# Optimization experiments

Measured on AMD Instinct MI355X. Metric: run time of the kernel, lower is better.

Reference implementation:

```python
import jax, jax.numpy as jnp
import numpy as np

B, T, C = 2, 2048, 1024
NH, HS = 16, 64  # n_heads, head_size; NH*HS == C


def setup_inputs() -> dict:
    key = jax.random.key(0)
    k1, k2, k3 = jax.random.split(key, 3)
    x = jax.random.normal(k1, (B, T, C), dtype=jnp.float32)
    W_attn = jax.random.normal(k2, (C, 3 * C), dtype=jnp.float32) * (C ** -0.5)
    b_attn = jax.random.normal(k3, (3 * C,), dtype=jnp.float32) * 0.02
    return {"x": x, "W_attn": W_attn, "b_attn": b_attn}


def reference(x, W_attn, b_attn):
    Bv, Tv, Cv = x.shape
    qkv = x @ W_attn + b_attn                       # [B,T,3C]
    q, k, v = jnp.split(qkv, 3, axis=-1)            # each [B,T,C]
    q = q.reshape(Bv, Tv, NH, HS)
    k = k.reshape(Bv, Tv, NH, HS)
    v = v.reshape(Bv, Tv, NH, HS)
    scale = HS ** -0.5
    wei = jnp.einsum('bqhd,bkhd->bhqk', q, k) * scale  # [B,H,T,T]
    causal = jnp.tril(jnp.ones((Tv, Tv), dtype=bool))
    wei = jnp.where(causal[None, None], wei, -jnp.inf)
    wei = jax.nn.softmax(wei, axis=-1)
    # dropout layers are identity in eval mode
    out = jnp.einsum('bhqk,bkhd->bqhd', wei, v)     # [B,T,H,HS]
    return out.reshape(Bv, Tv, Cv)
```

## Files before the change

### kernel.cpp

```cpp
#include <hip/hip_runtime.h>
#include <hip/hip_bf16.h>
#include <math.h>

#define BB   2
#define TT   2048
#define CC   1024
#define NH   16
#define HS   64
#define N3C  3072
#define MM   4096

typedef __attribute__((ext_vector_type(8))) short bf16x8;
typedef __attribute__((ext_vector_type(4))) float f32x4;

#define NINF (-__builtin_inff())
#define QSCALE 0.125f

__device__ __forceinline__ unsigned short f2bf(float f) {
    unsigned int u = __builtin_bit_cast(unsigned int, f);
    unsigned int r = u + 0x7fffu + ((u >> 16) & 1u);
    return (unsigned short)(r >> 16);
}

__device__ __forceinline__ unsigned short f2bf_fast(float f) {
    unsigned int u = __builtin_bit_cast(unsigned int, f);
    return (unsigned short)((u + 0x8000u) >> 16);
}

__device__ __forceinline__ void gl_lds16(const unsigned short* g, unsigned short* l) {
    __builtin_amdgcn_global_load_lds(
        (const __attribute__((address_space(1))) unsigned int*)g,
        (__attribute__((address_space(3))) unsigned int*)l, 16, 0, 0);
}

__global__ __launch_bounds__(256) void k_cast(const float* __restrict__ x,
                                              unsigned short* __restrict__ xb) {
    int i = (blockIdx.x * 256 + threadIdx.x) * 4;
    float4 v = *(const float4*)(x + i);
    ushort4 o;
    o.x = f2bf(v.x); o.y = f2bf(v.y); o.z = f2bf(v.z); o.w = f2bf(v.w);
    *(ushort4*)(xb + i) = o;
}

__global__ __launch_bounds__(256) void k_transpose_w(const float* __restrict__ W,
                                                     unsigned short* __restrict__ Wt) {
    __shared__ float tile[32][33];
    const int n0 = blockIdx.x * 32;
    const int k0 = blockIdx.y * 32;
    const int t = threadIdx.x;
    {
        int kr = t >> 3, ns = (t & 7) * 4;
        float4 v = *(const float4*)(W + (size_t)(k0 + kr) * N3C + n0 + ns);
        tile[kr][ns + 0] = v.x; tile[kr][ns + 1] = v.y;
        tile[kr][ns + 2] = v.z; tile[kr][ns + 3] = v.w;
    }
    __syncthreads();
    {
        int nr = t >> 3, ks = (t & 7) * 4;
        ushort4 o;
        o.x = f2bf(tile[ks + 0][nr]);
        o.y = f2bf(tile[ks + 1][nr]);
        o.z = f2bf(tile[ks + 2][nr]);
        o.w = f2bf(tile[ks + 3][nr]);
        *(ushort4*)(Wt + (size_t)(n0 + nr) * CC + k0 + ks) = o;
    }
}

#define EPS 72

__global__ __launch_bounds__(256) void k_gemm_qkv(const unsigned short* __restrict__ xb,
                                                  const unsigned short* __restrict__ wt,
                                                  const float* __restrict__ bias,
                                                  unsigned short* __restrict__ qb,
                                                  unsigned short* __restrict__ kb,
                                                  unsigned short* __restrict__ vt) {
    __shared__ unsigned short sA[128 * 32];
    __shared__ unsigned short sB[128 * 32];
    __shared__ unsigned short sE[4 * 64 * EPS];
    const int t = threadIdx.x;
    const int wave = t >> 6, lane = t & 63;
    const int quad = lane >> 4, c16 = lane & 15;
    const int wm = wave >> 1, wn = wave & 1;
    const int m0 = blockIdx.y * 128;
    const int n0 = blockIdx.x * 128;
    const int sel = n0 >> 10;

    f32x4 acc[4][4];
#pragma unroll
    for (int i = 0; i < 4; ++i)
#pragma unroll
        for (int j = 0; j < 4; ++j) acc[i][j] = f32x4{0, 0, 0, 0};

    const int srow = wave * 16 + (lane >> 2);
    const int scol = (lane & 3) * 8;
    const unsigned short* gA = xb + (size_t)(m0 + srow) * CC + scol;
    const unsigned short* gB = wt + (size_t)(n0 + srow) * CC + scol;
    unsigned short* lA = sA + wave * 512 + lane * 8;
    unsigned short* lB = sB + wave * 512 + lane * 8;

    for (int k0 = 0; k0 < CC; k0 += 32) {
        __syncthreads();
        gl_lds16(gA + k0, lA);
        gl_lds16(gA + k0 + (size_t)64 * CC, lA + 2048);
        gl_lds16(gB + k0, lB);
        gl_lds16(gB + k0 + (size_t)64 * CC, lB + 2048);
        __syncthreads();
        bf16x8 a[4], b[4];
#pragma unroll
        for (int rt = 0; rt < 4; ++rt)
            a[rt] = *(const bf16x8*)(sA + (wm * 64 + rt * 16 + c16) * 32 + quad * 8);
#pragma unroll
        for (int ct = 0; ct < 4; ++ct)
            b[ct] = *(const bf16x8*)(sB + (wn * 64 + ct * 16 + c16) * 32 + quad * 8);
#pragma unroll
        for (int rt = 0; rt < 4; ++rt)
#pragma unroll
            for (int ct = 0; ct < 4; ++ct)
                acc[rt][ct] = __builtin_amdgcn_mfma_f32_16x16x32_bf16(b[ct], a[rt], acc[rt][ct], 0, 0, 0);
    }

    const int head = ((n0 + wn * 64) >> 6) & 15;
    const int bh = (m0 >> 11) * NH + head;
    const int tbase = (m0 & 2047) + wm * 64;
    if (sel < 2) {
        unsigned short* dst = (sel == 0) ? qb : kb;
        const float sc = (sel == 0) ? QSCALE : 1.0f;
        unsigned short* ew = sE + wave * (64 * EPS);
#pragma unroll
        for (int ct = 0; ct < 4; ++ct) {
            const float4 bv4 = *(const float4*)(bias + n0 + wn * 64 + ct * 16 + quad * 4);
            const int d0 = ct * 16 + quad * 4;
#pragma unroll
            for (int rt = 0; rt < 4; ++rt) {
                ushort4 pk;
                pk.x = f2bf((acc[rt][ct][0] + bv4.x) * sc);
                pk.y = f2bf((acc[rt][ct][1] + bv4.y) * sc);
                pk.z = f2bf((acc[rt][ct][2] + bv4.z) * sc);
                pk.w = f2bf((acc[rt][ct][3] + bv4.w) * sc);
                *(ushort4*)(ew + (rt * 16 + c16) * EPS + d0) = pk;
            }
        }
        const size_t gbase = ((size_t)bh * TT + tbase) * HS;
#pragma unroll
        for (int i = 0; i < 8; ++i) {
            const int trow = i * 8 + (lane >> 3);
            bf16x8 row = *(const bf16x8*)(ew + trow * EPS + (lane & 7) * 8);
            *(bf16x8*)(dst + gbase + (size_t)trow * HS + (lane & 7) * 8) = row;
        }
    } else {
#pragma unroll
        for (int ct = 0; ct < 4; ++ct) {
            const float4 bv4 = *(const float4*)(bias + n0 + wn * 64 + ct * 16 + quad * 4);
#pragma unroll
            for (int r = 0; r < 4; ++r) {
                const int d = ct * 16 + quad * 4 + r;
                const float bv = ((const float*)&bv4)[r];
#pragma unroll
                for (int rt = 0; rt < 4; ++rt) {
                    const int tt = tbase + rt * 16 + c16;
                    vt[((size_t)bh * HS + d) * TT + tt] = f2bf(acc[rt][ct][r] + bv);
                }
            }
        }
    }
}

#define SPP 72

__global__ __launch_bounds__(64) void k_attn(const unsigned short* __restrict__ qb,
                                             const unsigned short* __restrict__ kb,
                                             const unsigned short* __restrict__ vt,
                                             float* __restrict__ out) {
    __shared__ unsigned short sP[32 * SPP];

    const int lane = threadIdx.x;
    const int quad = lane >> 4, c16 = lane & 15;
    const int qblk = 63 - (int)(blockIdx.x >> 5);
    const int bh = blockIdx.x & 31;
    const int qw = qblk * 32;

    const unsigned short* Qp = qb + (size_t)bh * TT * HS;
    const unsigned short* Kp = kb + (size_t)bh * TT * HS;
    const unsigned short* Vp = vt + (size_t)bh * HS * TT;

    bf16x8 qf[2][2];
#pragma unroll
    for (int j = 0; j < 2; ++j)
#pragma unroll
        for (int ks = 0; ks < 2; ++ks)
            qf[j][ks] = *(const bf16x8*)(Qp + (size_t)(qw + j * 16 + c16) * HS + ks * 32 + quad * 8);

    f32x4 o[4][2];
#pragma unroll
    for (int dt = 0; dt < 4; ++dt)
#pragma unroll
        for (int j = 0; j < 2; ++j) o[dt][j] = f32x4{0, 0, 0, 0};
    float lsum[2] = {0.f, 0.f};

    const unsigned short* kbase = Kp + (size_t)c16 * HS + quad * 8;
    const unsigned short* vbase = Vp + (size_t)c16 * TT + quad * 8;
    const int kiters = qblk / 2 + 1;

    bf16x8 kA[4][2], kB[4][2];

    auto loadK = [&](bf16x8 (&kf)[4][2], int kb0) {
#pragma unroll
        for (int mt = 0; mt < 4; ++mt) {
            kf[mt][0] = *(const bf16x8*)(kbase + (size_t)(kb0 + mt * 16) * HS);
            kf[mt][1] = *(const bf16x8*)(kbase + (size_t)(kb0 + mt * 16) * HS + 32);
        }
    };

    auto tile = [&](bf16x8 (&kf)[4][2], int it) {
        const int kb0 = it * 64;
        bf16x8 vf[4][2];
#pragma unroll
        for (int dt = 0; dt < 4; ++dt) {
            vf[dt][0] = *(const bf16x8*)(vbase + (size_t)dt * 16 * TT + kb0);
            vf[dt][1] = *(const bf16x8*)(vbase + (size_t)dt * 16 * TT + kb0 + 32);
        }
        f32x4 s[4][2];
#pragma unroll
        for (int mt = 0; mt < 4; ++mt)
#pragma unroll
            for (int j = 0; j < 2; ++j) s[mt][j] = f32x4{0, 0, 0, 0};
#pragma unroll
        for (int mt = 0; mt < 4; ++mt)
#pragma unroll
            for (int j = 0; j < 2; ++j) {
                s[mt][j] = __builtin_amdgcn_mfma_f32_16x16x32_bf16(kf[mt][0], qf[j][0], s[mt][j], 0, 0, 0);
                s[mt][j] = __builtin_amdgcn_mfma_f32_16x16x32_bf16(kf[mt][1], qf[j][1], s[mt][j], 0, 0, 0);
            }
        const bool maskit = (it == kiters - 1);
#pragma unroll
        for (int j = 0; j < 2; ++j) {
            const int rowq = qw + j * 16 + c16;
            float l = 0.f;
#pragma unroll
            for (int mt = 0; mt < 4; ++mt) {
                float p0, p1, p2, p3;
                if (maskit) {
                    const int k = kb0 + mt * 16 + quad * 4;
                    p0 = __expf((k     <= rowq) ? s[mt][j][0] : NINF);
                    p1 = __expf((k + 1 <= rowq) ? s[mt][j][1] : NINF);
                    p2 = __expf((k + 2 <= rowq) ? s[mt][j][2] : NINF);
                    p3 = __expf((k + 3 <= rowq) ? s[mt][j][3] : NINF);
                } else {
                    p0 = __expf(s[mt][j][0]);
                    p1 = __expf(s[mt][j][1]);
                    p2 = __expf(s[mt][j][2]);
                    p3 = __expf(s[mt][j][3]);
                }
                l += (p0 + p1) + (p2 + p3);
                ushort4 pk;
                pk.x = f2bf_fast(p0); pk.y = f2bf_fast(p1);
                pk.z = f2bf_fast(p2); pk.w = f2bf_fast(p3);
                *(ushort4*)(sP + (j * 16 + c16) * SPP + mt * 16 + quad * 4) = pk;
            }
            lsum[j] += l;
        }
        bf16x8 pf[2][2];
#pragma unroll
        for (int j = 0; j < 2; ++j)
#pragma unroll
            for (int ks = 0; ks < 2; ++ks)
                pf[j][ks] = *(const bf16x8*)(sP + (j * 16 + c16) * SPP + ks * 32 + quad * 8);
#pragma unroll
        for (int dt = 0; dt < 4; ++dt)
#pragma unroll
            for (int j = 0; j < 2; ++j) {
                o[dt][j] = __builtin_amdgcn_mfma_f32_16x16x32_bf16(vf[dt][0], pf[j][0], o[dt][j], 0, 0, 0);
                o[dt][j] = __builtin_amdgcn_mfma_f32_16x16x32_bf16(vf[dt][1], pf[j][1], o[dt][j], 0, 0, 0);
            }
    };

    loadK(kA, 0);
    int it = 0;
    while (true) {
        if (it + 1 < kiters) loadK(kB, (it + 1) * 64);
        tile(kA, it);
        ++it; if (it >= kiters) break;
        if (it + 1 < kiters) loadK(kA, (it + 1) * 64);
        tile(kB, it);
        ++it; if (it >= kiters) break;
    }

#pragma unroll
    for (int j = 0; j < 2; ++j) {
        lsum[j] += __shfl_xor(lsum[j], 16);
        lsum[j] += __shfl_xor(lsum[j], 32);
    }

    const int b_ = bh >> 4, h_ = bh & 15;
#pragma unroll
    for (int j = 0; j < 2; ++j) {
        const float il = 1.0f / lsum[j];
        const int q = qw + j * 16 + c16;
        float* orow = out + ((size_t)(b_ * TT + q)) * CC + h_ * HS;
#pragma unroll
        for (int dt = 0; dt < 4; ++dt) {
            float4 w;
            w.x = o[dt][j][0] * il; w.y = o[dt][j][1] * il;
            w.z = o[dt][j][2] * il; w.w = o[dt][j][3] * il;
            *(float4*)(orow + dt * 16 + quad * 4) = w;
        }
    }
}

extern "C" void kernel_launch(void* const* d_in, const int* in_sizes, int n_in,
                              void* d_out, int out_size, void* d_ws, size_t ws_size,
                              hipStream_t stream) {
    const float* x    = (const float*)d_in[0];
    const float* W    = (const float*)d_in[1];
    const float* bias = (const float*)d_in[2];
    float* out = (float*)d_out;

    char* ws = (char*)d_ws;
    unsigned short* xb = (unsigned short*)(ws);
    unsigned short* wt = (unsigned short*)(ws + 8388608);
    unsigned short* qb = (unsigned short*)(ws + 8388608 + 6291456);
    unsigned short* kb = (unsigned short*)(ws + 8388608 + 6291456 + 8388608);
    unsigned short* vt = (unsigned short*)(ws + 8388608 + 6291456 + 2 * 8388608);

    k_cast<<<dim3(MM * CC / (256 * 4)), dim3(256), 0, stream>>>(x, xb);
    k_transpose_w<<<dim3(N3C / 32, CC / 32), dim3(256), 0, stream>>>(W, wt);
    k_gemm_qkv<<<dim3(N3C / 128, MM / 128), dim3(256), 0, stream>>>(xb, wt, bias, qb, kb, vt);
    k_attn<<<dim3(64 * 32), dim3(64), 0, stream>>>(qb, kb, vt, out);
}
```

Measured before the change: 187.2 us.

## Split attention key loop across four waves with shared-memory reduction

```diff
diff --git a/kernel.cpp b/kernel.cpp
--- a/kernel.cpp
+++ b/kernel.cpp
@@ -166,18 +166,22 @@
 }
 
 #define SPP 72
-
-__global__ __launch_bounds__(64) void k_attn(const unsigned short* __restrict__ qb,
-                                             const unsigned short* __restrict__ kb,
-                                             const unsigned short* __restrict__ vt,
-                                             float* __restrict__ out) {
-    __shared__ unsigned short sP[32 * SPP];
-
-    const int lane = threadIdx.x;
+#define AW  4
+
+__global__ __launch_bounds__(256) void k_attn(const unsigned short* __restrict__ qb,
+                                              const unsigned short* __restrict__ kb,
+                                              const unsigned short* __restrict__ vt,
+                                              float* __restrict__ out) {
+    __shared__ alignas(16) char smem[AW * 32 * SPP * 2];
+
+    const int tid = threadIdx.x;
+    const int wave = tid >> 6, lane = tid & 63;
     const int quad = lane >> 4, c16 = lane & 15;
     const int qblk = 63 - (int)(blockIdx.x >> 5);
     const int bh = blockIdx.x & 31;
     const int qw = qblk * 32;
+
+    unsigned short* sPw = (unsigned short*)smem + wave * (32 * SPP);
 
     const unsigned short* Qp = qb + (size_t)bh * TT * HS;
     const unsigned short* Kp = kb + (size_t)bh * TT * HS;
@@ -255,7 +259,7 @@
                 ushort4 pk;
                 pk.x = f2bf_fast(p0); pk.y = f2bf_fast(p1);
                 pk.z = f2bf_fast(p2); pk.w = f2bf_fast(p3);
-                *(ushort4*)(sP + (j * 16 + c16) * SPP + mt * 16 + quad * 4) = pk;
+                *(ushort4*)(sPw + (j * 16 + c16) * SPP + mt * 16 + quad * 4) = pk;
             }
             lsum[j] += l;
         }
@@ -264,7 +268,7 @@
         for (int j = 0; j < 2; ++j)
 #pragma unroll
             for (int ks = 0; ks < 2; ++ks)
-                pf[j][ks] = *(const bf16x8*)(sP + (j * 16 + c16) * SPP + ks * 32 + quad * 8);
+                pf[j][ks] = *(const bf16x8*)(sPw + (j * 16 + c16) * SPP + ks * 32 + quad * 8);
 #pragma unroll
         for (int dt = 0; dt < 4; ++dt)
 #pragma unroll
@@ -274,16 +278,53 @@
             }
     };
 
-    loadK(kA, 0);
-    int it = 0;
-    while (true) {
-        if (it + 1 < kiters) loadK(kB, (it + 1) * 64);
-        tile(kA, it);
-        ++it; if (it >= kiters) break;
-        if (it + 1 < kiters) loadK(kA, (it + 1) * 64);
-        tile(kB, it);
-        ++it; if (it >= kiters) break;
-    }
+    int it = wave;
+    if (it < kiters) {
+        loadK(kA, it * 64);
+        while (true) {
+            int nxt = it + AW;
+            if (nxt < kiters) loadK(kB, nxt * 64);
+            tile(kA, it);
+            it = nxt;
+            if (it >= kiters) break;
+            nxt = it + AW;
+            if (nxt < kiters) loadK(kA, nxt * 64);
+            tile(kB, it);
+            it = nxt;
+            if (it >= kiters) break;
+        }
+    }
+
+    __syncthreads();
+    float* red = (float*)smem;
+    auto dumpO = [&](int slot) {
+        float* d = red + (size_t)(slot * 64 + lane) * 36;
+#pragma unroll
+        for (int dt = 0; dt < 4; ++dt)
+#pragma unroll
+            for (int j = 0; j < 2; ++j)
+                *(f32x4*)(d + (dt * 2 + j) * 4) = o[dt][j];
+        d[32] = lsum[0]; d[33] = lsum[1];
+    };
+    auto addO = [&](int slot) {
+        const float* s = red + (size_t)(slot * 64 + lane) * 36;
+#pragma unroll
+        for (int dt = 0; dt < 4; ++dt)
+#pragma unroll
+            for (int j = 0; j < 2; ++j)
+                o[dt][j] += *(const f32x4*)(s + (dt * 2 + j) * 4);
+        lsum[0] += s[32]; lsum[1] += s[33];
+    };
+    if (wave == 1) dumpO(0);
+    else if (wave == 3) dumpO(1);
+    __syncthreads();
+    if (wave == 0) addO(0);
+    else if (wave == 2) addO(1);
+    __syncthreads();
+    if (wave == 2) dumpO(0);
+    __syncthreads();
+    if (wave != 0) return;
+    addO(0);
 
 #pragma unroll
     for (int j = 0; j < 2; ++j) {
@@ -325,5 +366,5 @@
     k_cast<<<dim3(MM * CC / (256 * 4)), dim3(256), 0, stream>>>(x, xb);
     k_transpose_w<<<dim3(N3C / 32, CC / 32), dim3(256), 0, stream>>>(W, wt);
     k_gemm_qkv<<<dim3(N3C / 128, MM / 128), dim3(256), 0, stream>>>(xb, wt, bias, qb, kb, vt);
-    k_attn<<<dim3(64 * 32), dim3(64), 0, stream>>>(qb, kb, vt, out);
-}
+    k_attn<<<dim3(64 * 32), dim3(256), 0, stream>>>(qb, kb, vt, out);
+}
```

Result: slower. 208.9 us (+11.6%).

## Share K/V tiles across four waves via swizzled LDS double buffering

Applied to the files above, without the earlier changes.

```diff
diff --git a/kernel.cpp b/kernel.cpp
--- a/kernel.cpp
+++ b/kernel.cpp
@@ -166,18 +166,25 @@
 }
 
 #define SPP 72
-
-__global__ __launch_bounds__(64) void k_attn(const unsigned short* __restrict__ qb,
-                                             const unsigned short* __restrict__ kb,
-                                             const unsigned short* __restrict__ vt,
-                                             float* __restrict__ out) {
-    __shared__ unsigned short sP[32 * SPP];
-
-    const int lane = threadIdx.x;
+#define AW  4
+
+__global__ __launch_bounds__(256) void k_attn(const unsigned short* __restrict__ qb,
+                                              const unsigned short* __restrict__ kb,
+                                              const unsigned short* __restrict__ vt,
+                                              float* __restrict__ out) {
+    __shared__ unsigned short sK[2][64 * 64];
+    __shared__ unsigned short sV[2][64 * 64];
+    __shared__ unsigned short sP[AW][32 * SPP];
+
+    const int tid = threadIdx.x;
+    const int wave = tid >> 6, lane = tid & 63;
     const int quad = lane >> 4, c16 = lane & 15;
-    const int qblk = 63 - (int)(blockIdx.x >> 5);
+    const int g = blockIdx.x >> 5;
+    const int qbk = 15 - g;
     const int bh = blockIdx.x & 31;
-    const int qw = qblk * 32;
+    const int qw = qbk * 128 + wave * 32;
+    const int qmax = qw + 31;
+    const int kiters = 2 * (qbk + 1);
 
     const unsigned short* Qp = qb + (size_t)bh * TT * HS;
     const unsigned short* Kp = kb + (size_t)bh * TT * HS;
@@ -197,28 +204,32 @@
         for (int j = 0; j < 2; ++j) o[dt][j] = f32x4{0, 0, 0, 0};
     float lsum[2] = {0.f, 0.f};
 
-    const unsigned short* kbase = Kp + (size_t)c16 * HS + quad * 8;
-    const unsigned short* vbase = Vp + (size_t)c16 * TT + quad * 8;
-    const int kiters = qblk / 2 + 1;
-
-    bf16x8 kA[4][2], kB[4][2];
-
-    auto loadK = [&](bf16x8 (&kf)[4][2], int kb0) {
-#pragma unroll
-        for (int mt = 0; mt < 4; ++mt) {
-            kf[mt][0] = *(const bf16x8*)(kbase + (size_t)(kb0 + mt * 16) * HS);
-            kf[mt][1] = *(const bf16x8*)(kbase + (size_t)(kb0 + mt * 16) * HS + 32);
+    unsigned short* sPw = sP[wave];
+
+    const int srow = tid >> 3;
+    const int ssc = tid & 7;
+    auto stage = [&](int buf, int kt) {
+        const int kb0 = kt * 64;
+#pragma unroll
+        for (int rnd = 0; rnd < 2; ++rnd) {
+            const int row = rnd * 32 + srow;
+            const int sl = ((ssc ^ (row & 7)) * 8);
+            gl_lds16(Kp + (size_t)(kb0 + row) * HS + sl, &sK[buf][rnd * 2048 + tid * 8]);
+            gl_lds16(Vp + (size_t)row * TT + kb0 + sl, &sV[buf][rnd * 2048 + tid * 8]);
         }
     };
 
-    auto tile = [&](bf16x8 (&kf)[4][2], int it) {
-        const int kb0 = it * 64;
-        bf16x8 vf[4][2];
-#pragma unroll
-        for (int dt = 0; dt < 4; ++dt) {
-            vf[dt][0] = *(const bf16x8*)(vbase + (size_t)dt * 16 * TT + kb0);
-            vf[dt][1] = *(const bf16x8*)(vbase + (size_t)dt * 16 * TT + kb0 + 32);
-        }
+    auto tile = [&](int buf, int kt) {
+        const int kb0 = kt * 64;
+        const unsigned short* Kb = sK[buf];
+        const unsigned short* Vb = sV[buf];
+        bf16x8 kf[4][2];
+#pragma unroll
+        for (int mt = 0; mt < 4; ++mt)
+#pragma unroll
+            for (int ks = 0; ks < 2; ++ks)
+                kf[mt][ks] = *(const bf16x8*)(Kb + (mt * 16 + c16) * 64 +
+                                              (((ks * 4 + quad) ^ (c16 & 7)) * 8));
         f32x4 s[4][2];
 #pragma unroll
         for (int mt = 0; mt < 4; ++mt)
@@ -231,7 +242,14 @@
                 s[mt][j] = __builtin_amdgcn_mfma_f32_16x16x32_bf16(kf[mt][0], qf[j][0], s[mt][j], 0, 0, 0);
                 s[mt][j] = __builtin_amdgcn_mfma_f32_16x16x32_bf16(kf[mt][1], qf[j][1], s[mt][j], 0, 0, 0);
             }
-        const bool maskit = (it == kiters - 1);
+        bf16x8 vf[4][2];
+#pragma unroll
+        for (int dt = 0; dt < 4; ++dt)
+#pragma unroll
+            for (int ks = 0; ks < 2; ++ks)
+                vf[dt][ks] = *(const bf16x8*)(Vb + (dt * 16 + c16) * 64 +
+                                              (((ks * 4 + quad) ^ (c16 & 7)) * 8));
+        const bool maskit = (kb0 + 63 > qw);
 #pragma unroll
         for (int j = 0; j < 2; ++j) {
             const int rowq = qw + j * 16 + c16;
@@ -255,7 +273,7 @@
                 ushort4 pk;
                 pk.x = f2bf_fast(p0); pk.y = f2bf_fast(p1);
                 pk.z = f2bf_fast(p2); pk.w = f2bf_fast(p3);
-                *(ushort4*)(sP + (j * 16 + c16) * SPP + mt * 16 + quad * 4) = pk;
+                *(ushort4*)(sPw + (j * 16 + c16) * SPP + mt * 16 + quad * 4) = pk;
             }
             lsum[j] += l;
         }
@@ -264,7 +282,7 @@
         for (int j = 0; j < 2; ++j)
 #pragma unroll
             for (int ks = 0; ks < 2; ++ks)
-                pf[j][ks] = *(const bf16x8*)(sP + (j * 16 + c16) * SPP + ks * 32 + quad * 8);
+                pf[j][ks] = *(const bf16x8*)(sPw + (j * 16 + c16) * SPP + ks * 32 + quad * 8);
 #pragma unroll
         for (int dt = 0; dt < 4; ++dt)
 #pragma unroll
@@ -274,15 +292,19 @@
             }
     };
 
-    loadK(kA, 0);
-    int it = 0;
-    while (true) {
-        if (it + 1 < kiters) loadK(kB, (it + 1) * 64);
-        tile(kA, it);
-        ++it; if (it >= kiters) break;
-        if (it + 1 < kiters) loadK(kA, (it + 1) * 64);
-        tile(kB, it);
-        ++it; if (it >= kiters) break;
+    stage(0, 0);
+    for (int kt = 0; kt < kiters; ++kt) {
+        if (kt + 1 < kiters) {
+            stage((kt + 1) & 1, kt + 1);
+            asm volatile("s_waitcnt vmcnt(4)" ::: "memory");
+        } else {
+            asm volatile("s_waitcnt vmcnt(0)" ::: "memory");
+        }
+        __builtin_amdgcn_s_barrier();
+        asm volatile("" ::: "memory");
+        if (kt * 64 <= qmax) tile(kt & 1, kt);
+        __builtin_amdgcn_s_barrier();
+        asm volatile("" ::: "memory");
     }
 
 #pragma unroll
@@ -325,5 +347,5 @@
     k_cast<<<dim3(MM * CC / (256 * 4)), dim3(256), 0, stream>>>(x, xb);
     k_transpose_w<<<dim3(N3C / 32, CC / 32), dim3(256), 0, stream>>>(W, wt);
     k_gemm_qkv<<<dim3(N3C / 128, MM / 128), dim3(256), 0, stream>>>(xb, wt, bias, qb, kb, vt);
-    k_attn<<<dim3(64 * 32), dim3(64), 0, stream>>>(qb, kb, vt, out);
-}
+    k_attn<<<dim3(16 * 32), dim3(256), 0, stream>>>(qb, kb, vt, out);
+}
```

New measurement: 179.2 us. 4.3% less time.
